# Optimization experiments

Hardware: AMD Instinct MI355X
Metric: run time of the kernel (lower is better)

Reference implementation:

```python
import jax, jax.numpy as jnp
import numpy as np

B, S, H, NH, PF, L = 2, 2048, 1024, 16, 4096, 6
HD = H // NH
EPS = 1e-5


def setup_inputs() -> dict:
    key = jax.random.key(0)
    ks = jax.random.split(key, 12)
    s = lambda k, shp, fan: jax.random.normal(k, shp, jnp.float32) * (1.0 / np.sqrt(fan))
    return {
        "input_tensor": jax.random.normal(ks[0], (B, S, H), jnp.float32),
        "pos_emb": s(ks[1], (S, H), H),
        "Wq": s(ks[2], (L, H, H), H), "bq": jnp.zeros((L, H), jnp.float32),
        "Wk": s(ks[3], (L, H, H), H), "bk": jnp.zeros((L, H), jnp.float32),
        "Wv": s(ks[4], (L, H, H), H), "bv": jnp.zeros((L, H), jnp.float32),
        "Wo": s(ks[5], (L, H, H), H), "bo": jnp.zeros((L, H), jnp.float32),
        "ln_g": jnp.ones((L, H), jnp.float32), "ln_b": jnp.zeros((L, H), jnp.float32),
        "W1": s(ks[6], (L, H, PF), H), "b1": jnp.zeros((L, PF), jnp.float32),
        "W2": s(ks[7], (L, PF, H), PF), "b2": jnp.zeros((L, H), jnp.float32),
    }


def _layernorm(x, g, b):
    mu = jnp.mean(x, axis=-1, keepdims=True)
    var = jnp.mean(jnp.square(x - mu), axis=-1, keepdims=True)
    return (x - mu) * jax.lax.rsqrt(var + EPS) * g + b


def _encoder(input_tensor, pos_emb, params):
    # pos embed: same positions for every batch row
    src = input_tensor * jnp.sqrt(jnp.float32(H)) + pos_emb[None, :, :]

    def layer(src, p):
        Wq, bq, Wk, bk, Wv, bv, Wo, bo, g, b, W1, b1, W2, b2 = p
        q = (src @ Wq + bq).reshape(B, S, NH, HD)
        k = (src @ Wk + bk).reshape(B, S, NH, HD)
        v = (src @ Wv + bv).reshape(B, S, NH, HD)
        # scores [B, NH, S, S]
        energy = jnp.einsum("bqhd,bkhd->bhqk", q, k) / jnp.sqrt(jnp.float32(HD))
        attn = jax.nn.softmax(energy, axis=-1)
        ctx = jnp.einsum("bhqk,bkhd->bqhd", attn, v).reshape(B, S, H)
        attn_out = ctx @ Wo + bo
        src = _layernorm(src + attn_out, g, b)
        ffn = jax.nn.relu(src @ W1 + b1) @ W2 + b2
        src = _layernorm(src + ffn, g, b)  # same LayerNorm reused, as in source
        return src, None

    src, _ = jax.lax.scan(layer, src, params)
    return src


def reference(input_tensor, pos_emb, Wq, bq, Wk, bk, Wv, bv, Wo, bo, ln_g, ln_b, W1, b1, W2, b2):
    params = (Wq, bq, Wk, bk, Wv, bv, Wo, bo, ln_g, ln_b, W1, b1, W2, b2)
    return _encoder(input_tensor, pos_emb, params)
```

## Files before the change

### kernel.cpp

```cpp
#include <hip/hip_runtime.h>
#include <cstdint>

constexpr int Bc = 2, Sc = 2048, Hc = 1024, NHc = 16, HDc = 64, PFc = 4096, Lc = 6;
constexpr float EPSc = 1e-5f;
constexpr float QSC = 0.18033688011112042f;

using f32x4  = __attribute__((ext_vector_type(4))) float;
using bf16x8 = __attribute__((ext_vector_type(8))) __bf16;
using bf16x4 = __attribute__((ext_vector_type(4))) __bf16;
using u32x4  = __attribute__((ext_vector_type(4))) unsigned;

#if __has_builtin(__builtin_amdgcn_exp2f)
#define EXP2(x) __builtin_amdgcn_exp2f(x)
#else
#define EXP2(x) exp2f(x)
#endif

__device__ __forceinline__ f32x4 mfma16(bf16x8 a, bf16x8 b, f32x4 c) {
    return __builtin_amdgcn_mfma_f32_16x16x32_bf16(a, b, c, 0, 0, 0);
}

__device__ __forceinline__ void gload_lds16(const void* g, void* l) {
    __builtin_amdgcn_global_load_lds(
        (__attribute__((address_space(1))) void*)(uintptr_t)g,
        (__attribute__((address_space(3))) void*)(uint32_t)(uintptr_t)l,
        16, 0, 0);
}

struct HL { __bf16 h, l; };
__device__ __forceinline__ HL split2(float v) {
    HL r;
    r.h = (__bf16)v;
    r.l = (__bf16)(v - (float)r.h);
    return r;
}

__device__ __forceinline__ unsigned bfbits(__bf16 x) {
    return (unsigned)__builtin_bit_cast(unsigned short, x);
}
__device__ __forceinline__ unsigned packbf(float a, float b) {
    return bfbits((__bf16)a) | (bfbits((__bf16)b) << 16);
}

__global__ __launch_bounds__(256) void wconv_kernel(
    const float* __restrict__ in, __bf16* __restrict__ out, int K, int N)
{
    __shared__ float tile[64][65];
    const int t = threadIdx.x;
    const size_t lstride = (size_t)K * N;
    const float* ip = in + (size_t)blockIdx.z * lstride;
    __bf16* op = out + (size_t)blockIdx.z * lstride;
    const int n0 = blockIdx.x * 64, k0 = blockIdx.y * 64;
    #pragma unroll
    for (int c = 0; c < 4; ++c) {
        int idx = c * 256 + t;
        int row = idx >> 4;
        int c4  = idx & 15;
        float4 v = *(const float4*)(ip + (size_t)(k0 + row) * N + n0 + c4 * 4);
        tile[row][c4 * 4 + 0] = v.x; tile[row][c4 * 4 + 1] = v.y;
        tile[row][c4 * 4 + 2] = v.z; tile[row][c4 * 4 + 3] = v.w;
    }
    __syncthreads();
    #pragma unroll
    for (int c = 0; c < 4; ++c) {
        int idx = c * 256 + t;
        int n  = idx >> 4;
        int k4 = idx & 15;
        bf16x4 hh = { (__bf16)tile[k4 * 4 + 0][n], (__bf16)tile[k4 * 4 + 1][n],
                      (__bf16)tile[k4 * 4 + 2][n], (__bf16)tile[k4 * 4 + 3][n] };
        *(bf16x4*)(op + (size_t)(n0 + n) * K + k0 + k4 * 4) = hh;
    }
}

__global__ __launch_bounds__(256) void embed_kernel(
    const float* __restrict__ in, const float* __restrict__ pos,
    float* __restrict__ sf, __bf16* __restrict__ sh, __bf16* __restrict__ sl)
{
    const int n4 = (Bc * Sc * Hc) / 4;
    const int pmask = (Sc * Hc / 4) - 1;
    for (int i = blockIdx.x * 256 + threadIdx.x; i < n4; i += gridDim.x * 256) {
        float4 a = ((const float4*)in)[i];
        float4 p = ((const float4*)pos)[i & pmask];
        float4 r;
        r.x = a.x * 32.f + p.x; r.y = a.y * 32.f + p.y;
        r.z = a.z * 32.f + p.z; r.w = a.w * 32.f + p.w;
        ((float4*)sf)[i] = r;
        HL e0 = split2(r.x), e1 = split2(r.y), e2 = split2(r.z), e3 = split2(r.w);
        bf16x4 hh = { e0.h, e1.h, e2.h, e3.h };
        bf16x4 ll = { e0.l, e1.l, e2.l, e3.l };
        ((bf16x4*)sh)[i] = hh;
        ((bf16x4*)sl)[i] = ll;
    }
}

template<int BM, int OUTMODE, bool RELU>
__global__ __launch_bounds__(256) void gemm_bt_kernel(
    const __bf16* __restrict__ A, const __bf16* __restrict__ Wt,
    const float* __restrict__ bias, void* __restrict__ out,
    int M, int N, int K)
{
    constexpr int MI = BM / 32;
    __shared__ alignas(16) __bf16 Alds[2][BM * 64];
    __shared__ alignas(16) __bf16 Blds[2][128 * 64];

    const int tid = threadIdx.x, lane = tid & 63, wave = tid >> 6;
    const int lr = lane & 15, lg = lane >> 4;
    const int m0 = blockIdx.y * BM, n0 = blockIdx.x * 128;
    const int wm = (wave >> 1) * (BM / 2), wn = (wave & 1) * 64;

    f32x4 acc[MI][4] = {};

    auto stage = [&](int k0, int buf) {
        #pragma unroll
        for (int c = 0; c < BM / 32; ++c) {
            int li = c * 256 + tid;
            int row = li >> 3;
            int lcb = ((li & 7) << 4) ^ ((row & 7) << 4);
            gload_lds16(A + (size_t)(m0 + row) * K + k0 + (lcb >> 1),
                        (char*)Alds[buf] + (size_t)(c * 256 + wave * 64) * 16);
        }
        #pragma unroll
        for (int c = 0; c < 4; ++c) {
            int li = c * 256 + tid;
            int row = li >> 3;
            int lcb = ((li & 7) << 4) ^ ((row & 7) << 4);
            gload_lds16(Wt + (size_t)(n0 + row) * K + k0 + (lcb >> 1),
                        (char*)Blds[buf] + (size_t)(c * 256 + wave * 64) * 16);
        }
    };

    stage(0, 0);
    __syncthreads();
    int cur = 0;

    for (int k0 = 0; k0 < K; k0 += 64) {
        if (k0 + 64 < K) stage(k0 + 64, cur ^ 1);

        bf16x8 af[2][MI], bfr[2][4];
        #pragma unroll
        for (int ks = 0; ks < 2; ++ks) {
            #pragma unroll
            for (int i = 0; i < MI; ++i) {
                int ra = wm + i * 16 + lr;
                int pa = (ks * 64 + lg * 16) ^ ((ra & 7) << 4);
                af[ks][i] = *(const bf16x8*)((const char*)Alds[cur] + ra * 128 + pa);
            }
            #pragma unroll
            for (int i = 0; i < 4; ++i) {
                int rb = wn + i * 16 + lr;
                int pb = (ks * 64 + lg * 16) ^ ((rb & 7) << 4);
                bfr[ks][i] = *(const bf16x8*)((const char*)Blds[cur] + rb * 128 + pb);
            }
        }
        #pragma unroll
        for (int ks = 0; ks < 2; ++ks)
            #pragma unroll
            for (int mi = 0; mi < MI; ++mi)
                #pragma unroll
                for (int ni = 0; ni < 4; ++ni)
                    acc[mi][ni] = mfma16(af[ks][mi], bfr[ks][ni], acc[mi][ni]);

        __syncthreads();
        cur ^= 1;
    }

    #pragma unroll
    for (int ni = 0; ni < 4; ++ni) {
        int col = n0 + wn + ni * 16 + lr;
        float bv = bias[col];
        #pragma unroll
        for (int mi = 0; mi < MI; ++mi) {
            int rowb = m0 + wm + mi * 16 + lg * 4;
            #pragma unroll
            for (int r = 0; r < 4; ++r) {
                float v = acc[mi][ni][r] + bv;
                if (RELU) v = fmaxf(v, 0.f);
                size_t idx = (size_t)(rowb + r) * N + col;
                if constexpr (OUTMODE == 0) ((float*)out)[idx] = v;
                else                        ((__bf16*)out)[idx] = (__bf16)v;
            }
        }
    }
}

struct QKVBT {
    const __bf16 *wq, *wk, *wv;
    const float *bq, *bk, *bv;
    __bf16 *q, *k, *v;
};

__global__ __launch_bounds__(256) void qkv_bt_kernel(
    const __bf16* __restrict__ A, QKVBT a)
{
    constexpr int N = Hc, K = Hc;
    __shared__ alignas(16) __bf16 Alds[2][128 * 64];
    __shared__ alignas(16) __bf16 Blds[2][128 * 64];

    const int tid = threadIdx.x, lane = tid & 63, wave = tid >> 6;
    const int lr = lane & 15, lg = lane >> 4;
    const int gx = blockIdx.x;
    const int widx = gx >> 3;
    const int n0 = (gx & 7) * 128;
    const int m0 = blockIdx.y * 128;
    const int wm = (wave >> 1) * 64, wn = (wave & 1) * 64;

    const __bf16* Wt  = (widx == 0) ? a.wq : (widx == 1) ? a.wk : a.wv;
    const float* bias = (widx == 0) ? a.bq : (widx == 1) ? a.bk : a.bv;

    f32x4 acc[4][4] = {};

    auto stage = [&](int k0, int buf) {
        #pragma unroll
        for (int c = 0; c < 4; ++c) {
            int li = c * 256 + tid;
            int row = li >> 3;
            int lcb = ((li & 7) << 4) ^ ((row & 7) << 4);
            gload_lds16(A + (size_t)(m0 + row) * K + k0 + (lcb >> 1),
                        (char*)Alds[buf] + (size_t)(c * 256 + wave * 64) * 16);
            gload_lds16(Wt + (size_t)(n0 + row) * K + k0 + (lcb >> 1),
                        (char*)Blds[buf] + (size_t)(c * 256 + wave * 64) * 16);
        }
    };

    stage(0, 0);
    __syncthreads();
    int cur = 0;

    for (int k0 = 0; k0 < K; k0 += 64) {
        if (k0 + 64 < K) stage(k0 + 64, cur ^ 1);

        bf16x8 af[2][4], bfr[2][4];
        #pragma unroll
        for (int ks = 0; ks < 2; ++ks) {
            #pragma unroll
            for (int i = 0; i < 4; ++i) {
                int ra = wm + i * 16 + lr;
                int pa = (ks * 64 + lg * 16) ^ ((ra & 7) << 4);
                af[ks][i] = *(const bf16x8*)((const char*)Alds[cur] + ra * 128 + pa);
                int rb = wn + i * 16 + lr;
                int pb = (ks * 64 + lg * 16) ^ ((rb & 7) << 4);
                bfr[ks][i] = *(const bf16x8*)((const char*)Blds[cur] + rb * 128 + pb);
            }
        }
        #pragma unroll
        for (int ks = 0; ks < 2; ++ks)
            #pragma unroll
            for (int mi = 0; mi < 4; ++mi)
                #pragma unroll
                for (int ni = 0; ni < 4; ++ni)
                    acc[mi][ni] = mfma16(af[ks][mi], bfr[ks][ni], acc[mi][ni]);

        __syncthreads();
        cur ^= 1;
    }

    __bf16* outp = (widx == 0) ? a.q : (widx == 1) ? a.k : a.v;
    const float osc = (widx == 0) ? QSC : 1.f;
    #pragma unroll
    for (int ni = 0; ni < 4; ++ni) {
        int col = n0 + wn + ni * 16 + lr;
        float bv = bias[col];
        int hh = col >> 6, d = col & 63;
        #pragma unroll
        for (int mi = 0; mi < 4; ++mi) {
            int rowb = m0 + wm + mi * 16 + lg * 4;
            #pragma unroll
            for (int r = 0; r < 4; ++r) {
                int row = rowb + r;
                int bb = row >> 11, s = row & (Sc - 1);
                outp[((size_t)(bb * NHc + hh) * Sc + s) * HDc + d] =
                    (__bf16)((acc[mi][ni][r] + bv) * osc);
            }
        }
    }
}

struct QKVArgs {
    const float *Wq, *Wk, *Wv, *bq, *bk, *bv;
    __bf16 *qh, *ql, *kh, *kl, *vv;
};

__global__ __launch_bounds__(256) void qkv0_kernel(
    const __bf16* __restrict__ Ahi, const __bf16* __restrict__ Alo, QKVArgs a)
{
    constexpr int N = Hc, K = Hc;
    __shared__ alignas(16) __bf16 AldsH[128 * 64];
    __shared__ alignas(16) __bf16 AldsL[128 * 64];
    __shared__ alignas(16) __bf16 BldsH[128 * 64];
    __shared__ alignas(16) __bf16 BldsL[128 * 64];

    const int tid  = threadIdx.x;
    const int lane = tid & 63;
    const int wave = tid >> 6;
    const int lr   = lane & 15;
    const int lg   = lane >> 4;
    const int gx   = blockIdx.x;
    const int widx = gx >> 3;
    const int n0   = (gx & 7) * 128;
    const int m0   = blockIdx.y * 128;
    const int wm   = (wave >> 1) * 64;
    const int wn   = (wave & 1) * 64;
    const int bn   = tid & 127;
    const int bkh  = (tid >> 7) * 32;

    const float* Bw   = (widx == 0) ? a.Wq : (widx == 1) ? a.Wk : a.Wv;
    const float* bias = (widx == 0) ? a.bq : (widx == 1) ? a.bk : a.bv;

    f32x4 acc[4][4] = {};
    const float* bsrc0 = Bw + (size_t)bkh * N + n0 + bn;

    for (int k0 = 0; k0 < K; k0 += 64) {
        #pragma unroll
        for (int c = 0; c < 4; ++c) {
            int li  = c * 256 + tid;
            int row = li >> 3;
            int lcb = ((li & 7) << 4) ^ ((row & 7) << 4);
            size_t goff = (size_t)(m0 + row) * K + k0 + (lcb >> 1);
            size_t loff = (size_t)(c * 256 + wave * 64) * 16;
            gload_lds16(Ahi + goff, (char*)AldsH + loff);
            gload_lds16(Alo + goff, (char*)AldsL + loff);
        }
        const float* bs = bsrc0 + (size_t)k0 * N;
        #pragma unroll
        for (int c = 0; c < 4; ++c) {
            bf16x8 ph, plv;
            #pragma unroll
            for (int j = 0; j < 8; ++j) {
                HL e = split2(bs[(size_t)(c * 8 + j) * N]);
                ph[j] = e.h;
                plv[j] = e.l;
            }
            int pcb = (bkh * 2 + c * 16) ^ ((bn & 7) << 4);
            *(bf16x8*)((char*)BldsH + bn * 128 + pcb) = ph;
            *(bf16x8*)((char*)BldsL + bn * 128 + pcb) = plv;
        }
        __syncthreads();

        bf16x8 ah[2][4], al[2][4], bh[2][4], bl[2][4];
        #pragma unroll
        for (int ks = 0; ks < 2; ++ks) {
            #pragma unroll
            for (int i = 0; i < 4; ++i) {
                int ra = wm + i * 16 + lr;
                int pa = (ks * 64 + lg * 16) ^ ((ra & 7) << 4);
                ah[ks][i] = *(const bf16x8*)((const char*)AldsH + ra * 128 + pa);
                al[ks][i] = *(const bf16x8*)((const char*)AldsL + ra * 128 + pa);
                int rb = wn + i * 16 + lr;
                int pb = (ks * 64 + lg * 16) ^ ((rb & 7) << 4);
                bh[ks][i] = *(const bf16x8*)((const char*)BldsH + rb * 128 + pb);
                bl[ks][i] = *(const bf16x8*)((const char*)BldsL + rb * 128 + pb);
            }
        }
        #pragma unroll
        for (int ks = 0; ks < 2; ++ks)
            #pragma unroll
            for (int mi = 0; mi < 4; ++mi)
                #pragma unroll
                for (int ni = 0; ni < 4; ++ni) {
                    acc[mi][ni] = mfma16(ah[ks][mi], bh[ks][ni], acc[mi][ni]);
                    acc[mi][ni] = mfma16(al[ks][mi], bh[ks][ni], acc[mi][ni]);
                    acc[mi][ni] = mfma16(ah[ks][mi], bl[ks][ni], acc[mi][ni]);
                }
        __syncthreads();
    }

    __bf16* outh = (widx == 0) ? a.qh : (widx == 1) ? a.kh : a.vv;
    __bf16* outl = (widx == 0) ? a.ql : a.kl;
    const float osc = (widx == 0) ? QSC : 1.f;
    #pragma unroll
    for (int ni = 0; ni < 4; ++ni) {
        int col = n0 + wn + ni * 16 + lr;
        float bv = bias[col];
        int hh = col >> 6, d = col & 63;
        #pragma unroll
        for (int mi = 0; mi < 4; ++mi) {
            int rowb = m0 + wm + mi * 16 + lg * 4;
            #pragma unroll
            for (int r = 0; r < 4; ++r) {
                int row = rowb + r;
                int bb = row >> 11, s = row & (Sc - 1);
                size_t idx = ((size_t)(bb * NHc + hh) * Sc + s) * HDc + d;
                float v = (acc[mi][ni][r] + bv) * osc;
                if (widx < 2) {
                    HL e = split2(v);
                    outh[idx] = e.h;
                    outl[idx] = e.l;
                } else {
                    outh[idx] = (__bf16)v;
                }
            }
        }
    }
}

template<int QKSPLIT>
__global__ __launch_bounds__(256) void attn_kernel(
    const __bf16* __restrict__ Qh, const __bf16* __restrict__ Ql,
    const __bf16* __restrict__ Kh, const __bf16* __restrict__ Kl,
    const __bf16* __restrict__ V, __bf16* __restrict__ O)
{
    __shared__ alignas(16) __bf16 Ksh[2][64 * 64];
    __shared__ alignas(16) __bf16 Klo[QKSPLIT ? 2 : 1][QKSPLIT ? 64 * 64 : 8];
    __shared__ alignas(16) __bf16 VT[2][64 * 64];

    const int tid = threadIdx.x;
    const int lane = tid & 63, wave = tid >> 6;
    const int lr = lane & 15, lg = lane >> 4;
    const int h = blockIdx.y, b = blockIdx.z;
    const int q0 = blockIdx.x * 64 + wave * 16;

    const size_t headoff = ((size_t)b * NHc + h) * Sc * HDc;
    const __bf16* Qb  = Qh + headoff;
    const __bf16* Kb  = Kh + headoff;
    const __bf16* Klb = QKSPLIT ? (Kl + headoff) : nullptr;
    const __bf16* Vb  = V + headoff;

    const size_t qrow = (size_t)(q0 + lr) * HDc;
    bf16x8 qf0 = *(const bf16x8*)(Qb + qrow + lg * 8);
    bf16x8 qf1 = *(const bf16x8*)(Qb + qrow + 32 + lg * 8);
    bf16x8 qlo0, qlo1;
    if constexpr (QKSPLIT) {
        const __bf16* Qlb = Ql + headoff;
        qlo0 = *(const bf16x8*)(Qlb + qrow + lg * 8);
        qlo1 = *(const bf16x8*)(Qlb + qrow + 32 + lg * 8);
    }

    const int kp = tid & 31, dblk = tid >> 5;
    const int sp = (kp & 0x11) | ((kp & 0x06) << 1) | ((kp & 0x08) >> 2);

    auto stageK = [&](int kt, int buf) {
        #pragma unroll
        for (int c = 0; c < 2; ++c) {
            int li  = c * 256 + tid;
            int row = li >> 3;
            int lcb = ((li & 7) << 4) ^ ((row & 7) << 4);
            size_t goff = (size_t)(kt * 64 + row) * HDc + (lcb >> 1);
            size_t loff = (size_t)(c * 256 + wave * 64) * 16;
            gload_lds16(Kb + goff, (char*)Ksh[buf] + loff);
            if constexpr (QKSPLIT)
                gload_lds16(Klb + goff, (char*)Klo[buf] + loff);
        }
    };
    auto loadV = [&](int kt, bf16x8& va, bf16x8& vb2) {
        const __bf16* vs = Vb + (size_t)(kt * 64 + 2 * kp) * HDc + dblk * 8;
        va  = *(const bf16x8*)vs;
        vb2 = *(const bf16x8*)(vs + HDc);
    };
    auto writeVT = [&](int buf, bf16x8 va, bf16x8 vb2) {
        #pragma unroll
        for (int j = 0; j < 8; ++j) {
            int d = dblk * 8 + j;
            unsigned u = bfbits(va[j]) | (bfbits(vb2[j]) << 16);
            int byte = d * 128 + ((sp * 4) ^ ((d & 7) << 4));
            *(unsigned*)((char*)VT[buf] + byte) = u;
        }
    };

    f32x4 o[4] = {};
    float m = -1e30f, lsum = 0.f;

    stageK(0, 0);
    {
        bf16x8 va, vb2;
        loadV(0, va, vb2);
        writeVT(0, va, vb2);
    }
    __syncthreads();

    int cur = 0;
    for (int kt = 0; kt < Sc / 64; ++kt) {
        const int nb = cur ^ 1;
        const bool pf = (kt + 1 < Sc / 64);
        bf16x8 va, vb2;
        if (pf) {
            stageK(kt + 1, nb);
            loadV(kt + 1, va, vb2);
        }

        const char* Kc = (const char*)Ksh[cur];
        const char* Klc = (const char*)Klo[QKSPLIT ? cur : 0];
        f32x4 s[4];
        #pragma unroll
        for (int kg = 0; kg < 4; ++kg) {
            int ra = kg * 16 + lr;
            int pa0 = (lg * 16) ^ ((ra & 7) << 4);
            int pa1 = (64 + lg * 16) ^ ((ra & 7) << 4);
            bf16x8 kf0 = *(const bf16x8*)(Kc + ra * 128 + pa0);
            bf16x8 kf1 = *(const bf16x8*)(Kc + ra * 128 + pa1);
            f32x4 t = {};
            t = mfma16(kf0, qf0, t);
            t = mfma16(kf1, qf1, t);
            if constexpr (QKSPLIT) {
                bf16x8 kg0 = *(const bf16x8*)(Klc + ra * 128 + pa0);
                bf16x8 kg1 = *(const bf16x8*)(Klc + ra * 128 + pa1);
                t = mfma16(kg0, qf0, t);
                t = mfma16(kg1, qf1, t);
                t = mfma16(kf0, qlo0, t);
                t = mfma16(kf1, qlo1, t);
            }
            s[kg] = t;
        }

        float mt = -1e30f;
        #pragma unroll
        for (int kg = 0; kg < 4; ++kg)
            #pragma unroll
            for (int r = 0; r < 4; ++r)
                mt = fmaxf(mt, s[kg][r]);
        mt = fmaxf(mt, __shfl_xor(mt, 16));
        mt = fmaxf(mt, __shfl_xor(mt, 32));
        if (!__all(mt <= m + 8.f)) {
            float mnew = fmaxf(m, mt);
            float fac = EXP2(m - mnew);
            m = mnew;
            lsum *= fac;
            #pragma unroll
            for (int r = 0; r < 4; ++r) {
                float fr = __shfl(fac, (lg << 4) | (lg * 4 + r));
                #pragma unroll
                for (int nd = 0; nd < 4; ++nd) o[nd][r] *= fr;
            }
        }
        float ps = 0.f;
        #pragma unroll
        for (int kg = 0; kg < 4; ++kg)
            #pragma unroll
            for (int r = 0; r < 4; ++r) {
                float p = EXP2(s[kg][r] - m);
                ps += p;
                s[kg][r] = p;
            }
        ps += __shfl_xor(ps, 16);
        ps += __shfl_xor(ps, 32);
        lsum += ps;

        #pragma unroll
        for (int kh2 = 0; kh2 < 2; ++kh2) {
            u32x4 pk;
            pk[0] = packbf(s[2 * kh2][0],     s[2 * kh2][1]);
            pk[1] = packbf(s[2 * kh2][2],     s[2 * kh2][3]);
            pk[2] = packbf(s[2 * kh2 + 1][0], s[2 * kh2 + 1][1]);
            pk[3] = packbf(s[2 * kh2 + 1][2], s[2 * kh2 + 1][3]);
            bf16x8 paf = __builtin_bit_cast(bf16x8, pk);
            #pragma unroll
            for (int nd = 0; nd < 4; ++nd) {
                int d = nd * 16 + lr;
                int byte = d * 128 + ((64 * kh2 + 16 * lg) ^ ((d & 7) << 4));
                bf16x8 vbf = *(const bf16x8*)((const char*)VT[cur] + byte);
                o[nd] = mfma16(paf, vbf, o[nd]);
            }
        }

        if (pf) writeVT(nb, va, vb2);
        __syncthreads();
        cur = nb;
    }

    #pragma unroll
    for (int r = 0; r < 4; ++r) {
        float lv  = __shfl(lsum, (lg << 4) | (lg * 4 + r));
        float inv = 1.f / lv;
        size_t orow = ((size_t)b * Sc + q0 + lg * 4 + r) * Hc + h * HDc;
        #pragma unroll
        for (int nd = 0; nd < 4; ++nd)
            O[orow + nd * 16 + lr] = (__bf16)(o[nd][r] * inv);
    }
}

__global__ __launch_bounds__(256) void ln_kernel(
    const float* __restrict__ xr, const __bf16* __restrict__ y,
    const float* __restrict__ g, const float* __restrict__ beta,
    float* __restrict__ of, __bf16* __restrict__ oh)
{
    __shared__ float red[2][4];
    const int row = blockIdx.x, t = threadIdx.x;
    const int lane = t & 63, wave = t >> 6;
    const int idx = row * 256 + t;
    float4 a = ((const float4*)xr)[idx];
    bf16x4 cb = ((const bf16x4*)y)[idx];
    float4 v;
    v.x = a.x + (float)cb[0]; v.y = a.y + (float)cb[1];
    v.z = a.z + (float)cb[2]; v.w = a.w + (float)cb[3];
    float s1 = v.x + v.y + v.z + v.w;
    float s2 = v.x * v.x + v.y * v.y + v.z * v.z + v.w * v.w;
    #pragma unroll
    for (int off = 1; off < 64; off <<= 1) {
        s1 += __shfl_xor(s1, off);
        s2 += __shfl_xor(s2, off);
    }
    if (lane == 0) { red[0][wave] = s1; red[1][wave] = s2; }
    __syncthreads();
    s1 = red[0][0] + red[0][1] + red[0][2] + red[0][3];
    s2 = red[1][0] + red[1][1] + red[1][2] + red[1][3];
    const float mu   = s1 * (1.f / Hc);
    const float var  = s2 * (1.f / Hc) - mu * mu;
    const float rstd = rsqrtf(var + EPSc);
    float4 gg = ((const float4*)g)[t];
    float4 bb = ((const float4*)beta)[t];
    float4 r;
    r.x = (v.x - mu) * rstd * gg.x + bb.x;
    r.y = (v.y - mu) * rstd * gg.y + bb.y;
    r.z = (v.z - mu) * rstd * gg.z + bb.z;
    r.w = (v.w - mu) * rstd * gg.w + bb.w;
    ((float4*)of)[idx] = r;
    bf16x4 hh = { (__bf16)r.x, (__bf16)r.y, (__bf16)r.z, (__bf16)r.w };
    ((bf16x4*)oh)[idx] = hh;
}

extern "C" void kernel_launch(void* const* d_in, const int* in_sizes, int n_in,
                              void* d_out, int out_size, void* d_ws, size_t ws_size,
                              hipStream_t stream)
{
    const float* inp = (const float*)d_in[0];
    const float* pos = (const float*)d_in[1];
    const float* Wq  = (const float*)d_in[2];
    const float* bq  = (const float*)d_in[3];
    const float* Wk  = (const float*)d_in[4];
    const float* bk  = (const float*)d_in[5];
    const float* Wv  = (const float*)d_in[6];
    const float* bv  = (const float*)d_in[7];
    const float* Wo  = (const float*)d_in[8];
    const float* bo  = (const float*)d_in[9];
    const float* lng = (const float*)d_in[10];
    const float* lnb = (const float*)d_in[11];
    const float* W1  = (const float*)d_in[12];
    const float* b1  = (const float*)d_in[13];
    const float* W2  = (const float*)d_in[14];
    const float* b2  = (const float*)d_in[15];

    char* ws = (char*)d_ws;
    const size_t MB = 1u << 20;
    float*  src_f = (float*)(ws);
    __bf16* src_h = (__bf16*)(ws + 16 * MB);
    __bf16* src_l = (__bf16*)(ws + 24 * MB);
    __bf16* qh    = (__bf16*)(ws + 32 * MB);
    __bf16* kh    = (__bf16*)(ws + 40 * MB);
    __bf16* vv    = (__bf16*)(ws + 48 * MB);
    __bf16* ctx   = (__bf16*)(ws + 56 * MB);
    __bf16* ql    = (__bf16*)(ws + 64 * MB);
    __bf16* kl    = (__bf16*)(ws + 72 * MB);
    __bf16* tmpb  = (__bf16*)(ws + 80 * MB);
    __bf16* h1    = (__bf16*)(ws + 32 * MB);
    __bf16* wqT   = (__bf16*)(ws + 96 * MB);
    __bf16* wkT   = (__bf16*)(ws + 108 * MB);
    __bf16* wvT   = (__bf16*)(ws + 120 * MB);
    __bf16* woT   = (__bf16*)(ws + 132 * MB);
    __bf16* w1T   = (__bf16*)(ws + 144 * MB);
    __bf16* w2T   = (__bf16*)(ws + 192 * MB);

    const int M = Bc * Sc;

    wconv_kernel<<<dim3(16, 16, 6), 256, 0, stream>>>(Wq, wqT, Hc, Hc);
    wconv_kernel<<<dim3(16, 16, 6), 256, 0, stream>>>(Wk, wkT, Hc, Hc);
    wconv_kernel<<<dim3(16, 16, 6), 256, 0, stream>>>(Wv, wvT, Hc, Hc);
    wconv_kernel<<<dim3(16, 16, 6), 256, 0, stream>>>(Wo, woT, Hc, Hc);
    wconv_kernel<<<dim3(64, 16, 6), 256, 0, stream>>>(W1, w1T, Hc, PFc);
    wconv_kernel<<<dim3(16, 64, 6), 256, 0, stream>>>(W2, w2T, PFc, Hc);

    embed_kernel<<<2048, 256, 0, stream>>>(inp, pos, src_f, src_h, src_l);

    for (int l = 0; l < Lc; ++l) {
        const size_t wHH = (size_t)l * Hc * Hc;
        const size_t wH  = (size_t)l * Hc;
        if (l == 0) {
            QKVArgs qa = { Wq, Wk, Wv, bq, bk, bv, qh, ql, kh, kl, vv };
            qkv0_kernel<<<dim3(24, 32), 256, 0, stream>>>(src_h, src_l, qa);
            attn_kernel<1><<<dim3(32, 16, 2), 256, 0, stream>>>(qh, ql, kh, kl, vv, ctx);
        } else {
            QKVBT qa = { wqT + wHH, wkT + wHH, wvT + wHH, bq + wH, bk + wH, bv + wH,
                         qh, kh, vv };
            qkv_bt_kernel<<<dim3(24, 32), 256, 0, stream>>>(src_h, qa);
            attn_kernel<0><<<dim3(32, 16, 2), 256, 0, stream>>>(qh, nullptr, kh, nullptr, vv, ctx);
        }
        gemm_bt_kernel<64, 1, false><<<dim3(8, 64), 256, 0, stream>>>(
            ctx, woT + wHH, bo + wH, tmpb, M, Hc, Hc);
        ln_kernel<<<M, 256, 0, stream>>>(src_f, tmpb, lng + wH, lnb + wH, src_f, src_h);
        gemm_bt_kernel<128, 1, true><<<dim3(32, 32), 256, 0, stream>>>(
            src_h, w1T + (size_t)l * Hc * PFc, b1 + (size_t)l * PFc, h1, M, PFc, Hc);
        gemm_bt_kernel<64, 1, false><<<dim3(8, 64), 256, 0, stream>>>(
            h1, w2T + (size_t)l * PFc * Hc, b2 + wH, tmpb, M, Hc, PFc);
        float* dst = (l == Lc - 1) ? (float*)d_out : src_f;
        ln_kernel<<<M, 256, 0, stream>>>(src_f, tmpb, lng + wH, lnb + wH, dst, src_h);
    }
}
```

Measured before the change: 1.707 ms.

## Process two 16-row query tiles per wave in attention to reuse K/V tiles

```diff
diff --git a/kernel.cpp b/kernel.cpp
--- a/kernel.cpp
+++ b/kernel.cpp
@@ -407,7 +407,7 @@
     const int lane = tid & 63, wave = tid >> 6;
     const int lr = lane & 15, lg = lane >> 4;
     const int h = blockIdx.y, b = blockIdx.z;
-    const int q0 = blockIdx.x * 64 + wave * 16;
+    const int q0 = blockIdx.x * 128 + wave * 32;
 
     const size_t headoff = ((size_t)b * NHc + h) * Sc * HDc;
     const __bf16* Qb  = Qh + headoff;
@@ -415,14 +415,19 @@
     const __bf16* Klb = QKSPLIT ? (Kl + headoff) : nullptr;
     const __bf16* Vb  = V + headoff;
 
-    const size_t qrow = (size_t)(q0 + lr) * HDc;
-    bf16x8 qf0 = *(const bf16x8*)(Qb + qrow + lg * 8);
-    bf16x8 qf1 = *(const bf16x8*)(Qb + qrow + 32 + lg * 8);
-    bf16x8 qlo0, qlo1;
+    const size_t qrowA = (size_t)(q0 + lr) * HDc;
+    const size_t qrowB = qrowA + 16 * HDc;
+    bf16x8 qfA0 = *(const bf16x8*)(Qb + qrowA + lg * 8);
+    bf16x8 qfA1 = *(const bf16x8*)(Qb + qrowA + 32 + lg * 8);
+    bf16x8 qfB0 = *(const bf16x8*)(Qb + qrowB + lg * 8);
+    bf16x8 qfB1 = *(const bf16x8*)(Qb + qrowB + 32 + lg * 8);
+    bf16x8 qlA0, qlA1, qlB0, qlB1;
     if constexpr (QKSPLIT) {
         const __bf16* Qlb = Ql + headoff;
-        qlo0 = *(const bf16x8*)(Qlb + qrow + lg * 8);
-        qlo1 = *(const bf16x8*)(Qlb + qrow + 32 + lg * 8);
+        qlA0 = *(const bf16x8*)(Qlb + qrowA + lg * 8);
+        qlA1 = *(const bf16x8*)(Qlb + qrowA + 32 + lg * 8);
+        qlB0 = *(const bf16x8*)(Qlb + qrowB + lg * 8);
+        qlB1 = *(const bf16x8*)(Qlb + qrowB + 32 + lg * 8);
     }
 
     const int kp = tid & 31, dblk = tid >> 5;
@@ -456,8 +461,8 @@
         }
     };
 
-    f32x4 o[4] = {};
-    float m = -1e30f, lsum = 0.f;
+    f32x4 oA[4] = {}, oB[4] = {};
+    float mA = -1e30f, mB = -1e30f, lsA = 0.f, lsB = 0.f;
 
     stageK(0, 0);
     {
@@ -479,7 +484,7 @@
 
         const char* Kc = (const char*)Ksh[cur];
         const char* Klc = (const char*)Klo[QKSPLIT ? cur : 0];
-        f32x4 s[4];
+        f32x4 sA[4], sB[4];
         #pragma unroll
         for (int kg = 0; kg < 4; ++kg) {
             int ra = kg * 16 + lr;
@@ -487,67 +492,102 @@
             int pa1 = (64 + lg * 16) ^ ((ra & 7) << 4);
             bf16x8 kf0 = *(const bf16x8*)(Kc + ra * 128 + pa0);
             bf16x8 kf1 = *(const bf16x8*)(Kc + ra * 128 + pa1);
-            f32x4 t = {};
-            t = mfma16(kf0, qf0, t);
-            t = mfma16(kf1, qf1, t);
+            f32x4 tA = {}, tB = {};
+            tA = mfma16(kf0, qfA0, tA);
+            tA = mfma16(kf1, qfA1, tA);
+            tB = mfma16(kf0, qfB0, tB);
+            tB = mfma16(kf1, qfB1, tB);
             if constexpr (QKSPLIT) {
                 bf16x8 kg0 = *(const bf16x8*)(Klc + ra * 128 + pa0);
                 bf16x8 kg1 = *(const bf16x8*)(Klc + ra * 128 + pa1);
-                t = mfma16(kg0, qf0, t);
-                t = mfma16(kg1, qf1, t);
-                t = mfma16(kf0, qlo0, t);
-                t = mfma16(kf1, qlo1, t);
-            }
-            s[kg] = t;
-        }
-
-        float mt = -1e30f;
+                tA = mfma16(kg0, qfA0, tA);
+                tA = mfma16(kg1, qfA1, tA);
+                tA = mfma16(kf0, qlA0, tA);
+                tA = mfma16(kf1, qlA1, tA);
+                tB = mfma16(kg0, qfB0, tB);
+                tB = mfma16(kg1, qfB1, tB);
+                tB = mfma16(kf0, qlB0, tB);
+                tB = mfma16(kf1, qlB1, tB);
+            }
+            sA[kg] = tA;
+            sB[kg] = tB;
+        }
+
+        float mtA = -1e30f, mtB = -1e30f;
         #pragma unroll
         for (int kg = 0; kg < 4; ++kg)
             #pragma unroll
-            for (int r = 0; r < 4; ++r)
-                mt = fmaxf(mt, s[kg][r]);
-        mt = fmaxf(mt, __shfl_xor(mt, 16));
-        mt = fmaxf(mt, __shfl_xor(mt, 32));
-        if (!__all(mt <= m + 8.f)) {
-            float mnew = fmaxf(m, mt);
-            float fac = EXP2(m - mnew);
-            m = mnew;
-            lsum *= fac;
+            for (int r = 0; r < 4; ++r) {
+                mtA = fmaxf(mtA, sA[kg][r]);
+                mtB = fmaxf(mtB, sB[kg][r]);
+            }
+        mtA = fmaxf(mtA, __shfl_xor(mtA, 16));
+        mtA = fmaxf(mtA, __shfl_xor(mtA, 32));
+        mtB = fmaxf(mtB, __shfl_xor(mtB, 16));
+        mtB = fmaxf(mtB, __shfl_xor(mtB, 32));
+        if (!__all(mtA <= mA)) {
+            float mnew = fmaxf(mA, mtA);
+            float fac = EXP2(mA - mnew);
+            mA = mnew;
+            lsA *= fac;
             #pragma unroll
             for (int r = 0; r < 4; ++r) {
                 float fr = __shfl(fac, (lg << 4) | (lg * 4 + r));
                 #pragma unroll
-                for (int nd = 0; nd < 4; ++nd) o[nd][r] *= fr;
-            }
-        }
-        float ps = 0.f;
+                for (int nd = 0; nd < 4; ++nd) oA[nd][r] *= fr;
+            }
+        }
+        if (!__all(mtB <= mB)) {
+            float mnew = fmaxf(mB, mtB);
+            float fac = EXP2(mB - mnew);
+            mB = mnew;
+            lsB *= fac;
+            #pragma unroll
+            for (int r = 0; r < 4; ++r) {
+                float fr = __shfl(fac, (lg << 4) | (lg * 4 + r));
+                #pragma unroll
+                for (int nd = 0; nd < 4; ++nd) oB[nd][r] *= fr;
+            }
+        }
+        float psA = 0.f, psB = 0.f;
         #pragma unroll
         for (int kg = 0; kg < 4; ++kg)
             #pragma unroll
             for (int r = 0; r < 4; ++r) {
-                float p = EXP2(s[kg][r] - m);
-                ps += p;
-                s[kg][r] = p;
-            }
-        ps += __shfl_xor(ps, 16);
-        ps += __shfl_xor(ps, 32);
-        lsum += ps;
+                float pA = EXP2(sA[kg][r] - mA);
+                float pB = EXP2(sB[kg][r] - mB);
+                psA += pA;
+                psB += pB;
+                sA[kg][r] = pA;
+                sB[kg][r] = pB;
+            }
+        psA += __shfl_xor(psA, 16);
+        psA += __shfl_xor(psA, 32);
+        psB += __shfl_xor(psB, 16);
+        psB += __shfl_xor(psB, 32);
+        lsA += psA;
+        lsB += psB;
 
         #pragma unroll
         for (int kh2 = 0; kh2 < 2; ++kh2) {
-            u32x4 pk;
-            pk[0] = packbf(s[2 * kh2][0],     s[2 * kh2][1]);
-            pk[1] = packbf(s[2 * kh2][2],     s[2 * kh2][3]);
-            pk[2] = packbf(s[2 * kh2 + 1][0], s[2 * kh2 + 1][1]);
-            pk[3] = packbf(s[2 * kh2 + 1][2], s[2 * kh2 + 1][3]);
-            bf16x8 paf = __builtin_bit_cast(bf16x8, pk);
+            u32x4 pkA, pkB;
+            pkA[0] = packbf(sA[2 * kh2][0],     sA[2 * kh2][1]);
+            pkA[1] = packbf(sA[2 * kh2][2],     sA[2 * kh2][3]);
+            pkA[2] = packbf(sA[2 * kh2 + 1][0], sA[2 * kh2 + 1][1]);
+            pkA[3] = packbf(sA[2 * kh2 + 1][2], sA[2 * kh2 + 1][3]);
+            pkB[0] = packbf(sB[2 * kh2][0],     sB[2 * kh2][1]);
+            pkB[1] = packbf(sB[2 * kh2][2],     sB[2 * kh2][3]);
+            pkB[2] = packbf(sB[2 * kh2 + 1][0], sB[2 * kh2 + 1][1]);
+            pkB[3] = packbf(sB[2 * kh2 + 1][2], sB[2 * kh2 + 1][3]);
+            bf16x8 pafA = __builtin_bit_cast(bf16x8, pkA);
+            bf16x8 pafB = __builtin_bit_cast(bf16x8, pkB);
             #pragma unroll
             for (int nd = 0; nd < 4; ++nd) {
                 int d = nd * 16 + lr;
                 int byte = d * 128 + ((64 * kh2 + 16 * lg) ^ ((d & 7) << 4));
                 bf16x8 vbf = *(const bf16x8*)((const char*)VT[cur] + byte);
-                o[nd] = mfma16(paf, vbf, o[nd]);
+                oA[nd] = mfma16(pafA, vbf, oA[nd]);
+                oB[nd] = mfma16(pafB, vbf, oB[nd]);
             }
         }
 
@@ -558,12 +598,17 @@
 
     #pragma unroll
     for (int r = 0; r < 4; ++r) {
-        float lv  = __shfl(lsum, (lg << 4) | (lg * 4 + r));
-        float inv = 1.f / lv;
-        size_t orow = ((size_t)b * Sc + q0 + lg * 4 + r) * Hc + h * HDc;
-        #pragma unroll
-        for (int nd = 0; nd < 4; ++nd)
-            O[orow + nd * 16 + lr] = (__bf16)(o[nd][r] * inv);
+        float lvA = __shfl(lsA, (lg << 4) | (lg * 4 + r));
+        float lvB = __shfl(lsB, (lg << 4) | (lg * 4 + r));
+        float invA = 1.f / lvA;
+        float invB = 1.f / lvB;
+        size_t orowA = ((size_t)b * Sc + q0 + lg * 4 + r) * Hc + h * HDc;
+        size_t orowB = orowA + (size_t)16 * Hc;
+        #pragma unroll
+        for (int nd = 0; nd < 4; ++nd) {
+            O[orowA + nd * 16 + lr] = (__bf16)(oA[nd][r] * invA);
+            O[orowB + nd * 16 + lr] = (__bf16)(oB[nd][r] * invB);
+        }
     }
 }
 
@@ -665,12 +710,12 @@
         if (l == 0) {
             QKVArgs qa = { Wq, Wk, Wv, bq, bk, bv, qh, ql, kh, kl, vv };
             qkv0_kernel<<<dim3(24, 32), 256, 0, stream>>>(src_h, src_l, qa);
-            attn_kernel<1><<<dim3(32, 16, 2), 256, 0, stream>>>(qh, ql, kh, kl, vv, ctx);
+            attn_kernel<1><<<dim3(16, 16, 2), 256, 0, stream>>>(qh, ql, kh, kl, vv, ctx);
         } else {
             QKVBT qa = { wqT + wHH, wkT + wHH, wvT + wHH, bq + wH, bk + wH, bv + wH,
                          qh, kh, vv };
             qkv_bt_kernel<<<dim3(24, 32), 256, 0, stream>>>(src_h, qa);
-            attn_kernel<0><<<dim3(32, 16, 2), 256, 0, stream>>>(qh, nullptr, kh, nullptr, vv, ctx);
+            attn_kernel<0><<<dim3(16, 16, 2), 256, 0, stream>>>(qh, nullptr, kh, nullptr, vv, ctx);
         }
         gemm_bt_kernel<64, 1, false><<<dim3(8, 64), 256, 0, stream>>>(
             ctx, woT + wHH, bo + wH, tmpb, M, Hc, Hc);
```

Measured after the change: 1.697 ms. No clear change (-0.6%).
